# Kernel tuning notes

Hardware: AMD Instinct MI355X
Metric: run time of the kernel (lower is better)

Reference implementation:

```python
import jax, jax.numpy as jnp
import numpy as np

N_SITES = 100000
GRID = 192
C_IN = 256
C_MID = 64
C_OUT = 256


def _build_neighbor_idx(rng):
    # unique active voxel coordinates in a GRID^3 volume
    flat = rng.choice(GRID ** 3, size=N_SITES, replace=False).astype(np.int64)
    coords = np.stack(np.unravel_index(flat, (GRID, GRID, GRID)), axis=1)  # [N,3]
    order = np.argsort(flat)
    flat_sorted = flat[order]
    offs = np.array([(dx, dy, dz) for dx in (-1, 0, 1) for dy in (-1, 0, 1) for dz in (-1, 0, 1)], dtype=np.int64)  # [27,3]
    nb = np.full((N_SITES, 27), N_SITES, dtype=np.int64)  # N_SITES = "missing" pad row
    for k in range(27):
        nc = coords + offs[k]
        valid = np.all((nc >= 0) & (nc < GRID), axis=1)
        nflat = nc[:, 0] * GRID * GRID + nc[:, 1] * GRID + nc[:, 2]
        pos = np.searchsorted(flat_sorted, nflat)
        pos_c = np.clip(pos, 0, N_SITES - 1)
        found = valid & (flat_sorted[pos_c] == nflat)
        nb[:, k] = np.where(found, order[pos_c], N_SITES)
    return nb


def setup_inputs() -> dict:
    key = jax.random.key(0)
    ks = jax.random.split(key, 8)
    rng = np.random.default_rng(0)
    neighbor_idx = jnp.asarray(_build_neighbor_idx(rng))  # [N,27] int
    features = jax.random.normal(ks[0], (N_SITES, C_IN), dtype=jnp.float32)
    # conv weights (scn convs have no bias here)
    W1 = jax.random.normal(ks[1], (C_IN, C_MID), dtype=jnp.float32) * 0.02   # 1x1x1 submanifold conv
    W2 = jax.random.normal(ks[2], (27, C_MID, C_MID), dtype=jnp.float32) * 0.02  # 3x3x3 submanifold conv
    W3 = jax.random.normal(ks[3], (C_MID, C_OUT), dtype=jnp.float32) * 0.02  # 1x1x1 submanifold conv
    # SparseAffineChannel3d: weight ~ U[0,1), bias = 0
    g1 = jax.random.uniform(ks[4], (C_MID,), dtype=jnp.float32)
    b1 = jnp.zeros((C_MID,), dtype=jnp.float32)
    g2 = jax.random.uniform(ks[5], (C_MID,), dtype=jnp.float32)
    b2 = jnp.zeros((C_MID,), dtype=jnp.float32)
    g3 = jax.random.uniform(ks[6], (C_OUT,), dtype=jnp.float32)
    b3 = jnp.zeros((C_OUT,), dtype=jnp.float32)
    return {"features": features, "W1": W1, "W2": W2, "W3": W3,
            "g1": g1, "b1": b1, "g2": g2, "b2": b2, "g3": g3, "b3": b3,
            "neighbor_idx": neighbor_idx}


def _submanifold_conv3(h, W2, neighbor_idx):
    # gather-GEMM: missing neighbors (index N_SITES) read the zero pad row
    h_pad = jnp.concatenate([h, jnp.zeros((1, h.shape[1]), dtype=h.dtype)], axis=0)
    gathered = h_pad[neighbor_idx]  # [N, 27, C_MID]
    return jnp.einsum('nkc,kcd->nd', gathered, W2)


def reference(features, W1, W2, W3, g1, b1, g2, b2, g3, b3, neighbor_idx):
    residual = features
    # conv1 (1x1x1 submanifold) + affine + relu
    out = features @ W1
    out = jax.nn.relu(out * g1 + b1)
    # conv2 (3x3x3 submanifold) + affine + relu
    out = _submanifold_conv3(out, W2, neighbor_idx)
    out = jax.nn.relu(out * g2 + b2)
    # conv3 (1x1x1 submanifold) + affine
    out = out @ W3
    out = out * g3 + b3
    # residual add + relu
    return jax.nn.relu(out + residual)
```

## Files before the change

### kernel.cpp

```cpp
#include <hip/hip_runtime.h>
#include <hip/hip_bf16.h>

#define N_SITES 100000
#define C_IN 256
#define C_MID 64
#define C_OUT 256

typedef __attribute__((ext_vector_type(8))) short bf16x8;
typedef __attribute__((ext_vector_type(4))) float f32x4;

__device__ inline short f2bf(float f) {
  return __builtin_bit_cast(short, __float2bfloat16(f));
}

__device__ inline f32x4 mfma16(bf16x8 a, bf16x8 b, f32x4 c) {
  return __builtin_amdgcn_mfma_f32_16x16x32_bf16(a, b, c, 0, 0, 0);
}

__global__ __launch_bounds__(256) void k_prep(const float* __restrict__ W1,
                                              const float* __restrict__ W2,
                                              const float* __restrict__ W3,
                                              short* __restrict__ W1T,
                                              short* __restrict__ W2T,
                                              short* __restrict__ W3T,
                                              short* __restrict__ h1) {
  int i = blockIdx.x * 256 + threadIdx.x;
  if (i < 16384) {
    int n = i >> 8, k = i & 255;
    W1T[i] = f2bf(W1[k * 64 + n]);
  } else if (i < 16384 + 110592) {
    int j = i - 16384;
    int k = j >> 12, rem = j & 4095;
    int dout = rem >> 6, din = rem & 63;
    W2T[j] = f2bf(W2[k * 4096 + din * 64 + dout]);
  } else if (i < 16384 + 110592 + 16384) {
    int j = i - (16384 + 110592);
    int n = j >> 6, k = j & 63;
    W3T[j] = f2bf(W3[k * 256 + n]);
  } else if (i < 16384 + 110592 + 16384 + 64) {
    h1[(size_t)N_SITES * 64 + (i - (16384 + 110592 + 16384))] = 0;
  }
}

__global__ __launch_bounds__(256, 4) void k_conv1(const float* __restrict__ F,
                                                  const short* __restrict__ W1T,
                                                  const float* __restrict__ g1,
                                                  const float* __restrict__ b1,
                                                  short* __restrict__ h1) {
  int tid = threadIdx.x;
  int lane = tid & 63, wave = tid >> 6;
  int l15 = lane & 15, l4 = lane >> 4;
  int base = blockIdx.x * 64 + wave * 16;

  int row = base + l15;
  int rowc = row < N_SITES ? row : (N_SITES - 1);
  const float* fr = F + (size_t)rowc * 256 + l4 * 8;

  float4 fa[16];
#pragma unroll
  for (int kk = 0; kk < 8; ++kk) {
    fa[2 * kk]     = *(const float4*)(fr + kk * 32);
    fa[2 * kk + 1] = *(const float4*)(fr + kk * 32 + 4);
  }

  f32x4 acc[4];
#pragma unroll
  for (int nf = 0; nf < 4; ++nf) acc[nf] = (f32x4){0.f, 0.f, 0.f, 0.f};

#pragma unroll
  for (int kk = 0; kk < 8; ++kk) {
    float4 a0 = fa[2 * kk], a1 = fa[2 * kk + 1];
    bf16x8 af;
    af[0] = f2bf(a0.x); af[1] = f2bf(a0.y); af[2] = f2bf(a0.z); af[3] = f2bf(a0.w);
    af[4] = f2bf(a1.x); af[5] = f2bf(a1.y); af[6] = f2bf(a1.z); af[7] = f2bf(a1.w);
#pragma unroll
    for (int nf = 0; nf < 4; ++nf) {
      bf16x8 bf = *(const bf16x8*)(W1T + (nf * 16 + l15) * 256 + kk * 32 + l4 * 8);
      acc[nf] = mfma16(af, bf, acc[nf]);
    }
  }

#pragma unroll
  for (int nf = 0; nf < 4; ++nf) {
    int col = nf * 16 + l15;
    float g = g1[col], bb = b1[col];
#pragma unroll
    for (int r = 0; r < 4; ++r) {
      int site = base + l4 * 4 + r;
      if (site < N_SITES) {
        float v = fmaxf(acc[nf][r] * g + bb, 0.f);
        h1[(size_t)site * 64 + col] = f2bf(v);
      }
    }
  }
}

__global__ __launch_bounds__(128) void k_conv2(const short* __restrict__ h1,
                                               const short* __restrict__ W2T,
                                               const float* __restrict__ g2,
                                               const float* __restrict__ b2,
                                               const int* __restrict__ NB,
                                               short* __restrict__ h2) {
  __shared__ int nbt[128 * 27];
  int tid = threadIdx.x;

  int nwg = gridDim.x;
  int q = nwg >> 3, r = nwg & 7;
  int xcd = blockIdx.x & 7, idx = blockIdx.x >> 3;
  int swz = (xcd < r) ? (xcd * (q + 1) + idx)
                      : (r * (q + 1) + (xcd - r) * q + idx);
  int blockbase = swz * 128;

  for (int i = tid; i < 128 * 27; i += 128) {
    int site = blockbase + i / 27;
    nbt[i] = (site < N_SITES) ? NB[(size_t)site * 27 + (i % 27)] : N_SITES;
  }
  __syncthreads();

  int lane = tid & 63, wave = tid >> 6;
  int l15 = lane & 15, l4 = lane >> 4;
  int wrow = wave * 64 + l15;

  f32x4 acc[4][4];
#pragma unroll
  for (int mf = 0; mf < 4; ++mf)
#pragma unroll
    for (int nf = 0; nf < 4; ++nf) acc[mf][nf] = (f32x4){0.f, 0.f, 0.f, 0.f};

  bf16x8 bufA[4][2], bufB[4][2];

#define LOADBUF(BUF, KK)                                                    \
  {                                                                         \
    _Pragma("unroll")                                                       \
    for (int mf = 0; mf < 4; ++mf) {                                        \
      int n = nbt[(wrow + mf * 16) * 27 + (KK)];                            \
      const short* p = h1 + (size_t)n * 64 + l4 * 8;                        \
      BUF[mf][0] = *(const bf16x8*)p;                                       \
      BUF[mf][1] = *(const bf16x8*)(p + 32);                                \
    }                                                                       \
  }

#define COMPUTE(BUF, KK)                                                    \
  {                                                                         \
    const short* wk = W2T + (size_t)(KK) * 4096 + l15 * 64 + l4 * 8;        \
    _Pragma("unroll")                                                       \
    for (int nf = 0; nf < 4; ++nf) {                                        \
      bf16x8 b0 = *(const bf16x8*)(wk + nf * 1024);                         \
      bf16x8 b1 = *(const bf16x8*)(wk + nf * 1024 + 32);                    \
      _Pragma("unroll")                                                     \
      for (int mf = 0; mf < 4; ++mf) {                                      \
        acc[mf][nf] = mfma16(BUF[mf][0], b0, acc[mf][nf]);                  \
        acc[mf][nf] = mfma16(BUF[mf][1], b1, acc[mf][nf]);                  \
      }                                                                     \
    }                                                                       \
  }

  LOADBUF(bufA, 0);
  for (int k = 0; k < 26; k += 2) {
    LOADBUF(bufB, k + 1);
    COMPUTE(bufA, k);
    LOADBUF(bufA, (k + 2 < 27) ? k + 2 : 26);
    COMPUTE(bufB, k + 1);
  }
  COMPUTE(bufA, 26);

#undef LOADBUF
#undef COMPUTE

#pragma unroll
  for (int mf = 0; mf < 4; ++mf) {
#pragma unroll
    for (int nf = 0; nf < 4; ++nf) {
      int col = nf * 16 + l15;
      float g = g2[col], bb = b2[col];
#pragma unroll
      for (int rr = 0; rr < 4; ++rr) {
        int site = blockbase + wave * 64 + mf * 16 + l4 * 4 + rr;
        if (site < N_SITES) {
          float v = fmaxf(acc[mf][nf][rr] * g + bb, 0.f);
          h2[(size_t)site * 64 + col] = f2bf(v);
        }
      }
    }
  }
}

__global__ __launch_bounds__(256, 4) void k_conv3(const short* __restrict__ h2,
                                                  const short* __restrict__ W3T,
                                                  const float* __restrict__ g3,
                                                  const float* __restrict__ b3,
                                                  const float* __restrict__ F,
                                                  float* __restrict__ out) {
  int tid = threadIdx.x;
  int lane = tid & 63, wave = tid >> 6;
  int l15 = lane & 15, l4 = lane >> 4;
  int sbase = blockIdx.x * 64 + wave * 16;

  int site = sbase + l15;
  int sitec = site < N_SITES ? site : (N_SITES - 1);
  const short* pb = h2 + (size_t)sitec * 64 + l4 * 8;
  bf16x8 bv0 = *(const bf16x8*)pb;
  bf16x8 bv1 = *(const bf16x8*)(pb + 32);

  f32x4 acc[16];
#pragma unroll
  for (int nb = 0; nb < 16; ++nb) acc[nb] = (f32x4){0.f, 0.f, 0.f, 0.f};

#pragma unroll
  for (int nb = 0; nb < 16; ++nb) {
    const short* pa = W3T + (nb * 16 + l15) * 64 + l4 * 8;
    bf16x8 a0 = *(const bf16x8*)pa;
    bf16x8 a1 = *(const bf16x8*)(pa + 32);
    acc[nb] = mfma16(a0, bv0, acc[nb]);
    acc[nb] = mfma16(a1, bv1, acc[nb]);
  }

  if (site < N_SITES) {
#pragma unroll
    for (int nb = 0; nb < 16; ++nb) {
      int chan = nb * 16 + l4 * 4;
      size_t o = (size_t)site * 256 + chan;
      float4 g = *(const float4*)(g3 + chan);
      float4 bb = *(const float4*)(b3 + chan);
      float4 fv = *(const float4*)(F + o);
      float4 r;
      r.x = fmaxf(acc[nb][0] * g.x + bb.x + fv.x, 0.f);
      r.y = fmaxf(acc[nb][1] * g.y + bb.y + fv.y, 0.f);
      r.z = fmaxf(acc[nb][2] * g.z + bb.z + fv.z, 0.f);
      r.w = fmaxf(acc[nb][3] * g.w + bb.w + fv.w, 0.f);
      *(float4*)(out + o) = r;
    }
  }
}

extern "C" void kernel_launch(void* const* d_in, const int* in_sizes, int n_in,
                              void* d_out, int out_size, void* d_ws, size_t ws_size,
                              hipStream_t stream) {
  const float* F  = (const float*)d_in[0];
  const float* W1 = (const float*)d_in[1];
  const float* W2 = (const float*)d_in[2];
  const float* W3 = (const float*)d_in[3];
  const float* g1 = (const float*)d_in[4];
  const float* b1 = (const float*)d_in[5];
  const float* g2 = (const float*)d_in[6];
  const float* b2 = (const float*)d_in[7];
  const float* g3 = (const float*)d_in[8];
  const float* b3 = (const float*)d_in[9];
  const int*   NB = (const int*)d_in[10];
  float* out = (float*)d_out;

  char* ws = (char*)d_ws;
  short* W1T = (short*)(ws);
  short* W2T = (short*)(ws + 32768);
  short* W3T = (short*)(ws + 32768 + 221184);
  short* h1  = (short*)(ws + 32768 + 221184 + 32768);
  short* h2  = (short*)(ws + 32768 + 221184 + 32768 + 12800128);

  k_prep<<<dim3(561), dim3(256), 0, stream>>>(W1, W2, W3, W1T, W2T, W3T, h1);
  k_conv1<<<dim3((N_SITES + 63) / 64), dim3(256), 0, stream>>>(F, W1T, g1, b1, h1);
  k_conv2<<<dim3((N_SITES + 127) / 128), dim3(128), 0, stream>>>(h1, W2T, g2, b2, NB, h2);
  k_conv3<<<dim3((N_SITES + 63) / 64), dim3(256), 0, stream>>>(h2, W3T, g3, b3, F, out);
}
```

Measured before the change: 349.3 us.

## Split conv2 kernel-offset loop across waves and retile conv1/conv3 for reuse

conv2 now launches 256 threads per block, and the two wave pairs each handle half of the 27 neighbor offsets. The partial accumulators are summed through a shared-memory reduction before the affine/ReLU epilogue, which doubles the waves available to hide gather latency per tile. conv1 processes two 16-row fragments per wave so each W1 fragment load feeds two MFMAs. conv3 splits output channels across waves and keeps four site fragments per wave, so each W3 load is reused four times. In exchange, conv2 uses about 35KB more LDS and adds a barrier, which may reduce occupancy.

```diff
diff --git a/kernel.cpp b/kernel.cpp
--- a/kernel.cpp
+++ b/kernel.cpp
@@ -42,66 +42,72 @@
   }
 }
 
-__global__ __launch_bounds__(256, 4) void k_conv1(const float* __restrict__ F,
-                                                  const short* __restrict__ W1T,
-                                                  const float* __restrict__ g1,
-                                                  const float* __restrict__ b1,
-                                                  short* __restrict__ h1) {
+__global__ __launch_bounds__(256) void k_conv1(const float* __restrict__ F,
+                                               const short* __restrict__ W1T,
+                                               const float* __restrict__ g1,
+                                               const float* __restrict__ b1,
+                                               short* __restrict__ h1) {
   int tid = threadIdx.x;
   int lane = tid & 63, wave = tid >> 6;
   int l15 = lane & 15, l4 = lane >> 4;
-  int base = blockIdx.x * 64 + wave * 16;
-
-  int row = base + l15;
-  int rowc = row < N_SITES ? row : (N_SITES - 1);
-  const float* fr = F + (size_t)rowc * 256 + l4 * 8;
-
-  float4 fa[16];
+  int base = blockIdx.x * 128 + wave * 32;
+
+  int r0 = base + l15;       r0 = r0 < N_SITES ? r0 : (N_SITES - 1);
+  int r1 = base + 16 + l15;  r1 = r1 < N_SITES ? r1 : (N_SITES - 1);
+  const float* f0 = F + (size_t)r0 * 256 + l4 * 8;
+  const float* f1 = F + (size_t)r1 * 256 + l4 * 8;
+
+  f32x4 acc[2][4];
+#pragma unroll
+  for (int mf = 0; mf < 2; ++mf)
+#pragma unroll
+    for (int nf = 0; nf < 4; ++nf) acc[mf][nf] = (f32x4){0.f, 0.f, 0.f, 0.f};
+
 #pragma unroll
   for (int kk = 0; kk < 8; ++kk) {
-    fa[2 * kk]     = *(const float4*)(fr + kk * 32);
-    fa[2 * kk + 1] = *(const float4*)(fr + kk * 32 + 4);
-  }
-
-  f32x4 acc[4];
-#pragma unroll
-  for (int nf = 0; nf < 4; ++nf) acc[nf] = (f32x4){0.f, 0.f, 0.f, 0.f};
-
-#pragma unroll
-  for (int kk = 0; kk < 8; ++kk) {
-    float4 a0 = fa[2 * kk], a1 = fa[2 * kk + 1];
-    bf16x8 af;
-    af[0] = f2bf(a0.x); af[1] = f2bf(a0.y); af[2] = f2bf(a0.z); af[3] = f2bf(a0.w);
-    af[4] = f2bf(a1.x); af[5] = f2bf(a1.y); af[6] = f2bf(a1.z); af[7] = f2bf(a1.w);
+    float4 x00 = *(const float4*)(f0 + kk * 32);
+    float4 x01 = *(const float4*)(f0 + kk * 32 + 4);
+    float4 x10 = *(const float4*)(f1 + kk * 32);
+    float4 x11 = *(const float4*)(f1 + kk * 32 + 4);
+    bf16x8 a0, a1;
+    a0[0] = f2bf(x00.x); a0[1] = f2bf(x00.y); a0[2] = f2bf(x00.z); a0[3] = f2bf(x00.w);
+    a0[4] = f2bf(x01.x); a0[5] = f2bf(x01.y); a0[6] = f2bf(x01.z); a0[7] = f2bf(x01.w);
+    a1[0] = f2bf(x10.x); a1[1] = f2bf(x10.y); a1[2] = f2bf(x10.z); a1[3] = f2bf(x10.w);
+    a1[4] = f2bf(x11.x); a1[5] = f2bf(x11.y); a1[6] = f2bf(x11.z); a1[7] = f2bf(x11.w);
 #pragma unroll
     for (int nf = 0; nf < 4; ++nf) {
       bf16x8 bf = *(const bf16x8*)(W1T + (nf * 16 + l15) * 256 + kk * 32 + l4 * 8);
-      acc[nf] = mfma16(af, bf, acc[nf]);
-    }
-  }
-
-#pragma unroll
-  for (int nf = 0; nf < 4; ++nf) {
-    int col = nf * 16 + l15;
-    float g = g1[col], bb = b1[col];
-#pragma unroll
-    for (int r = 0; r < 4; ++r) {
-      int site = base + l4 * 4 + r;
-      if (site < N_SITES) {
-        float v = fmaxf(acc[nf][r] * g + bb, 0.f);
-        h1[(size_t)site * 64 + col] = f2bf(v);
+      acc[0][nf] = mfma16(a0, bf, acc[0][nf]);
+      acc[1][nf] = mfma16(a1, bf, acc[1][nf]);
+    }
+  }
+
+#pragma unroll
+  for (int mf = 0; mf < 2; ++mf) {
+#pragma unroll
+    for (int nf = 0; nf < 4; ++nf) {
+      int col = nf * 16 + l15;
+      float g = g1[col], bb = b1[col];
+#pragma unroll
+      for (int r = 0; r < 4; ++r) {
+        int site = base + mf * 16 + l4 * 4 + r;
+        if (site < N_SITES) {
+          float v = fmaxf(acc[mf][nf][r] * g + bb, 0.f);
+          h1[(size_t)site * 64 + col] = f2bf(v);
+        }
       }
     }
   }
 }
 
-__global__ __launch_bounds__(128) void k_conv2(const short* __restrict__ h1,
+__global__ __launch_bounds__(256) void k_conv2(const short* __restrict__ h1,
                                                const short* __restrict__ W2T,
                                                const float* __restrict__ g2,
                                                const float* __restrict__ b2,
                                                const int* __restrict__ NB,
                                                short* __restrict__ h2) {
   __shared__ int nbt[128 * 27];
+  __shared__ float red[128][68];
   int tid = threadIdx.x;
 
   int nwg = gridDim.x;
@@ -111,7 +117,7 @@
                       : (r * (q + 1) + (xcd - r) * q + idx);
   int blockbase = swz * 128;
 
-  for (int i = tid; i < 128 * 27; i += 128) {
+  for (int i = tid; i < 128 * 27; i += 256) {
     int site = blockbase + i / 27;
     nbt[i] = (site < N_SITES) ? NB[(size_t)site * 27 + (i % 27)] : N_SITES;
   }
@@ -119,7 +125,10 @@
 
   int lane = tid & 63, wave = tid >> 6;
   int l15 = lane & 15, l4 = lane >> 4;
-  int wrow = wave * 64 + l15;
+  int wlo = wave & 1, whi = wave >> 1;
+  int wrow = wlo * 64 + l15;
+  int kbeg = whi ? 13 : 0;
+  int kend = whi ? 27 : 13;
 
   f32x4 acc[4][4];
 #pragma unroll
@@ -155,80 +164,108 @@
     }                                                                       \
   }
 
-  LOADBUF(bufA, 0);
-  for (int k = 0; k < 26; k += 2) {
+  int k = kbeg;
+  LOADBUF(bufA, kbeg);
+  while (k + 2 <= kend) {
     LOADBUF(bufB, k + 1);
     COMPUTE(bufA, k);
-    LOADBUF(bufA, (k + 2 < 27) ? k + 2 : 26);
+    LOADBUF(bufA, (k + 2 < kend) ? k + 2 : k + 1);
     COMPUTE(bufB, k + 1);
-  }
-  COMPUTE(bufA, 26);
+    k += 2;
+  }
+  if (k < kend) COMPUTE(bufA, k);
 
 #undef LOADBUF
 #undef COMPUTE
 
-#pragma unroll
-  for (int mf = 0; mf < 4; ++mf) {
-#pragma unroll
-    for (int nf = 0; nf < 4; ++nf) {
-      int col = nf * 16 + l15;
-      float g = g2[col], bb = b2[col];
-#pragma unroll
-      for (int rr = 0; rr < 4; ++rr) {
-        int site = blockbase + wave * 64 + mf * 16 + l4 * 4 + rr;
-        if (site < N_SITES) {
-          float v = fmaxf(acc[mf][nf][rr] * g + bb, 0.f);
-          h2[(size_t)site * 64 + col] = f2bf(v);
+  if (whi) {
+#pragma unroll
+    for (int mf = 0; mf < 4; ++mf)
+#pragma unroll
+      for (int nf = 0; nf < 4; ++nf)
+#pragma unroll
+        for (int rr = 0; rr < 4; ++rr)
+          red[wlo * 64 + mf * 16 + l4 * 4 + rr][nf * 16 + l15] = acc[mf][nf][rr];
+  }
+  __syncthreads();
+  if (!whi) {
+#pragma unroll
+    for (int mf = 0; mf < 4; ++mf) {
+#pragma unroll
+      for (int nf = 0; nf < 4; ++nf) {
+        int col = nf * 16 + l15;
+        float g = g2[col], bb = b2[col];
+#pragma unroll
+        for (int rr = 0; rr < 4; ++rr) {
+          int row = wlo * 64 + mf * 16 + l4 * 4 + rr;
+          int site = blockbase + row;
+          if (site < N_SITES) {
+            float v = acc[mf][nf][rr] + red[row][col];
+            h2[(size_t)site * 64 + col] = f2bf(fmaxf(v * g + bb, 0.f));
+          }
         }
       }
     }
   }
 }
 
-__global__ __launch_bounds__(256, 4) void k_conv3(const short* __restrict__ h2,
-                                                  const short* __restrict__ W3T,
-                                                  const float* __restrict__ g3,
-                                                  const float* __restrict__ b3,
-                                                  const float* __restrict__ F,
-                                                  float* __restrict__ out) {
+__global__ __launch_bounds__(256) void k_conv3(const short* __restrict__ h2,
+                                               const short* __restrict__ W3T,
+                                               const float* __restrict__ g3,
+                                               const float* __restrict__ b3,
+                                               const float* __restrict__ F,
+                                               float* __restrict__ out) {
   int tid = threadIdx.x;
   int lane = tid & 63, wave = tid >> 6;
   int l15 = lane & 15, l4 = lane >> 4;
-  int sbase = blockIdx.x * 64 + wave * 16;
-
-  int site = sbase + l15;
-  int sitec = site < N_SITES ? site : (N_SITES - 1);
-  const short* pb = h2 + (size_t)sitec * 64 + l4 * 8;
-  bf16x8 bv0 = *(const bf16x8*)pb;
-  bf16x8 bv1 = *(const bf16x8*)(pb + 32);
-
-  f32x4 acc[16];
-#pragma unroll
-  for (int nb = 0; nb < 16; ++nb) acc[nb] = (f32x4){0.f, 0.f, 0.f, 0.f};
-
-#pragma unroll
-  for (int nb = 0; nb < 16; ++nb) {
-    const short* pa = W3T + (nb * 16 + l15) * 64 + l4 * 8;
+  int sbase = blockIdx.x * 64;
+
+  bf16x8 bv[4][2];
+#pragma unroll
+  for (int sf = 0; sf < 4; ++sf) {
+    int s = sbase + sf * 16 + l15;
+    s = s < N_SITES ? s : (N_SITES - 1);
+    const short* pb = h2 + (size_t)s * 64 + l4 * 8;
+    bv[sf][0] = *(const bf16x8*)pb;
+    bv[sf][1] = *(const bf16x8*)(pb + 32);
+  }
+
+  f32x4 acc[4][4];
+#pragma unroll
+  for (int cf = 0; cf < 4; ++cf)
+#pragma unroll
+    for (int sf = 0; sf < 4; ++sf) acc[cf][sf] = (f32x4){0.f, 0.f, 0.f, 0.f};
+
+#pragma unroll
+  for (int cf = 0; cf < 4; ++cf) {
+    const short* pa = W3T + (size_t)(wave * 64 + cf * 16 + l15) * 64 + l4 * 8;
     bf16x8 a0 = *(const bf16x8*)pa;
     bf16x8 a1 = *(const bf16x8*)(pa + 32);
-    acc[nb] = mfma16(a0, bv0, acc[nb]);
-    acc[nb] = mfma16(a1, bv1, acc[nb]);
-  }
-
-  if (site < N_SITES) {
-#pragma unroll
-    for (int nb = 0; nb < 16; ++nb) {
-      int chan = nb * 16 + l4 * 4;
-      size_t o = (size_t)site * 256 + chan;
-      float4 g = *(const float4*)(g3 + chan);
-      float4 bb = *(const float4*)(b3 + chan);
-      float4 fv = *(const float4*)(F + o);
-      float4 r;
-      r.x = fmaxf(acc[nb][0] * g.x + bb.x + fv.x, 0.f);
-      r.y = fmaxf(acc[nb][1] * g.y + bb.y + fv.y, 0.f);
-      r.z = fmaxf(acc[nb][2] * g.z + bb.z + fv.z, 0.f);
-      r.w = fmaxf(acc[nb][3] * g.w + bb.w + fv.w, 0.f);
-      *(float4*)(out + o) = r;
+#pragma unroll
+    for (int sf = 0; sf < 4; ++sf) {
+      acc[cf][sf] = mfma16(a0, bv[sf][0], acc[cf][sf]);
+      acc[cf][sf] = mfma16(a1, bv[sf][1], acc[cf][sf]);
+    }
+  }
+
+#pragma unroll
+  for (int cf = 0; cf < 4; ++cf) {
+    int chan = wave * 64 + cf * 16 + l4 * 4;
+    float4 g = *(const float4*)(g3 + chan);
+    float4 bb = *(const float4*)(b3 + chan);
+#pragma unroll
+    for (int sf = 0; sf < 4; ++sf) {
+      int site = sbase + sf * 16 + l15;
+      if (site < N_SITES) {
+        size_t o = (size_t)site * 256 + chan;
+        float4 fv = *(const float4*)(F + o);
+        float4 rr;
+        rr.x = fmaxf(acc[cf][sf][0] * g.x + bb.x + fv.x, 0.f);
+        rr.y = fmaxf(acc[cf][sf][1] * g.y + bb.y + fv.y, 0.f);
+        rr.z = fmaxf(acc[cf][sf][2] * g.z + bb.z + fv.z, 0.f);
+        rr.w = fmaxf(acc[cf][sf][3] * g.w + bb.w + fv.w, 0.f);
+        *(float4*)(out + o) = rr;
+      }
     }
   }
 }
@@ -257,7 +294,7 @@
   short* h2  = (short*)(ws + 32768 + 221184 + 32768 + 12800128);
 
   k_prep<<<dim3(561), dim3(256), 0, stream>>>(W1, W2, W3, W1T, W2T, W3T, h1);
-  k_conv1<<<dim3((N_SITES + 63) / 64), dim3(256), 0, stream>>>(F, W1T, g1, b1, h1);
-  k_conv2<<<dim3((N_SITES + 127) / 128), dim3(128), 0, stream>>>(h1, W2T, g2, b2, NB, h2);
+  k_conv1<<<dim3((N_SITES + 127) / 128), dim3(256), 0, stream>>>(F, W1T, g1, b1, h1);
+  k_conv2<<<dim3((N_SITES + 127) / 128), dim3(256), 0, stream>>>(h1, W2T, g2, b2, NB, h2);
   k_conv3<<<dim3((N_SITES + 63) / 64), dim3(256), 0, stream>>>(h2, W3T, g3, b3, F, out);
 }
```

After: 362.4 us. 3.7% more time.
